# Kernel tuning notes

Hardware: AMD Instinct MI355X
Metric: run time of the kernel (lower is better)

Reference implementation:

```python
import jax, jax.numpy as jnp
import numpy as np

# Hyperparameters (from HOIMLoss init_kwargs / defaults)
NUM_PIDS = 5532
NUM_CQ = 5000
NUM_BG = 5000
NUM_FEATURES = 256
BATCH = 4096
OIM_SCALAR = 30.0
ALPHA_D = 0.25
ALPHA_R = 0.25
GAMMA_D = 2.0
GAMMA_R = 2.0


def _l2norm(x):
    return x / jnp.maximum(jnp.linalg.norm(x, axis=-1, keepdims=True), 1e-12)


def setup_inputs() -> dict:
    key = jax.random.key(0)
    k1, k2, k3, k4, k5 = jax.random.split(key, 5)
    inputs = _l2norm(jax.random.normal(k1, (BATCH, NUM_FEATURES), dtype=jnp.float32))
    # roi_label: -2 = background, -1 = ignored unlabeled, [0, NUM_PIDS) = identity
    roi_label = jax.random.randint(k2, (BATCH,), -2, NUM_PIDS)
    lut = _l2norm(jax.random.normal(k3, (NUM_PIDS, NUM_FEATURES), dtype=jnp.float32))
    cq = _l2norm(jax.random.normal(k4, (NUM_CQ, NUM_FEATURES), dtype=jnp.float32))
    cqb = _l2norm(jax.random.normal(k5, (NUM_BG, NUM_FEATURES), dtype=jnp.float32))
    return {"inputs": inputs, "roi_label": roi_label, "lut": lut, "cq": cq, "cqb": cqb}


def reference(inputs, roi_label, lut, cq, cqb):
    # OIM2CQ.forward: concat([inputs@cqb.T, inputs@lut.T, inputs@cq.T], dim=1)
    table = jnp.concatenate([cqb, lut, cq], axis=0)        # [BG+P+CQ, F]
    projected = OIM_SCALAR * (inputs @ table.T)            # [B, BG+P+CQ]

    valid = roi_label >= -1      # non-background rows (inds in torch code)
    labeled = roi_label >= 0     # rows contributing to nll (ignore_index=-1)

    # OIM focal loss over non-background columns [labeled | unlabeled]
    proj_non_bg = projected[:, NUM_BG:]                    # [B, P+CQ]
    logp = jax.nn.log_softmax(proj_non_bg, axis=-1)
    p = jnp.exp(logp)
    focal_p = ALPHA_R * (1.0 - p) ** GAMMA_R * logp
    safe_lab = jnp.clip(roi_label, 0, NUM_PIDS - 1)
    row_loss = -jnp.take_along_axis(focal_p, safe_lab[:, None], axis=1)[:, 0]
    row_loss = jnp.where(labeled, row_loss, 0.0)           # ignore_index=-1 -> 0

    # Detection focal loss over (background, foreground) mass
    all_probs = jax.nn.softmax(projected, axis=-1)
    cls_score = jnp.stack(
        [all_probs[:, :NUM_BG].sum(axis=-1), all_probs[:, NUM_BG:].sum(axis=-1)],
        axis=-1,
    )                                                      # [B, 2]
    det_label = jnp.clip(roi_label + 2, 0, 1)              # -2 -> 0, else 1
    focal_det = ALPHA_D * (1.0 - cls_score) ** GAMMA_D * jnp.log(cls_score)
    loss_det = -jnp.take_along_axis(focal_det, det_label[:, None], axis=1)[:, 0].mean()

    # dynamic_lambda: weight per-row oim loss by detached fg prob squared
    cls_non_bg = jax.lax.stop_gradient(cls_score[:, 1])
    row_loss = row_loss * cls_non_bg ** 2
    n_valid = jnp.maximum(valid.sum(), 1).astype(projected.dtype)
    loss_oim = jnp.sum(jnp.where(valid, row_loss, 0.0)) / n_valid

    return cls_score, loss_det, loss_oim
```

## Files before the change

kernel.cpp:

```cpp
#include <hip/hip_runtime.h>
#include <hip/hip_bf16.h>

typedef unsigned short u16;
typedef __attribute__((ext_vector_type(8))) short bf16x8;
typedef __attribute__((ext_vector_type(4))) short bf16x4;
typedef __attribute__((ext_vector_type(4))) float f32x4;
typedef __attribute__((ext_vector_type(16))) float f32x16;

#define NBG   5000
#define NPID  5532
#define NTOT  15532
#define FEAT  256
#define BATCH 4096
#define SCALE_LOG2E 43.280851226668994f
#define LPITCH 264

#define BGPAD    5120
#define TOTPAD   15872
#define NCHUNKS  62
#define NTILE_B  992
#define TILE_SH  4096
#define NTILE_A  256
#define STEP_SH  8192
#define NB_LIMIT 15652

#define TABT_BYTES ((size_t)NTILE_B * TILE_SH * 2)
#define AT_BYTES   ((size_t)NTILE_A * TILE_SH * 2)
#define SUMS_OFF   (TABT_BYTES + AT_BYTES)
#define SUMS_FLOATS 8196
#define WS_NEED    (SUMS_OFF + SUMS_FLOATS * 4)

__device__ __forceinline__ float fexp2(float x) {
#if __has_builtin(__builtin_amdgcn_exp2f)
    return __builtin_amdgcn_exp2f(x);
#else
    return exp2f(x);
#endif
}

__device__ __forceinline__ void atomic_add_f(float* p, float v) {
    __hip_atomic_fetch_add(p, v, __ATOMIC_RELAXED, __HIP_MEMORY_SCOPE_AGENT);
}
__device__ __forceinline__ short f2bf(float f) {
    return (short)__bfloat16_as_ushort(__float2bfloat16(f));
}
__device__ __forceinline__ int swz(int rc, int q) { return q ^ ((rc >> 1) & 3); }

__device__ __forceinline__ const float* table_row(
    int n, const float* __restrict__ lut, const float* __restrict__ cq,
    const float* __restrict__ cqb)
{
    const int nc = n < NTOT ? n : NTOT - 1;
    if (nc < NBG)        return cqb + (size_t)nc * FEAT;
    if (nc < NBG + NPID) return lut + (size_t)(nc - NBG) * FEAT;
    return cq + (size_t)(nc - NBG - NPID) * FEAT;
}

#define TAB_UNITS (NTILE_B * 512)
#define A_UNITS   (NTILE_A * 512)
#define PRE_BLOCKS ((TAB_UNITS + A_UNITS) / 256)

__global__ __launch_bounds__(256) void prepass_kernel(
    const float* __restrict__ inputs, const float* __restrict__ lut,
    const float* __restrict__ cq, const float* __restrict__ cqb,
    u16* __restrict__ tabt, u16* __restrict__ at, float* __restrict__ S)
{
    const int u = blockIdx.x * 256 + threadIdx.x;
    if (u < SUMS_FLOATS) S[u] = 0.f;

    if (u < TAB_UNITS) {
        const int tile = u >> 9, v = u & 511;
        const int kk = v >> 6, col = (v >> 2) & 15, q = v & 3;
        const int cg = tile * 16 + col;
        const int srcn  = (cg < BGPAD) ? cg : cg - 120;
        const bool valid = (cg < BGPAD) ? (cg < NBG) : (cg < NB_LIMIT);
        bf16x8 r = {0, 0, 0, 0, 0, 0, 0, 0};
        if (valid) {
            const float* src = table_row(srcn, lut, cq, cqb) + kk * 32 + q * 8;
            const f32x4 lo = *(const f32x4*)src;
            const f32x4 hi = *(const f32x4*)(src + 4);
            r = bf16x8{ f2bf(lo[0] * SCALE_LOG2E), f2bf(lo[1] * SCALE_LOG2E),
                        f2bf(lo[2] * SCALE_LOG2E), f2bf(lo[3] * SCALE_LOG2E),
                        f2bf(hi[0] * SCALE_LOG2E), f2bf(hi[1] * SCALE_LOG2E),
                        f2bf(hi[2] * SCALE_LOG2E), f2bf(hi[3] * SCALE_LOG2E) };
        }
        const size_t off = (size_t)tile * TILE_SH + kk * 512 + col * 32 + swz(col, q) * 8;
        *(bf16x8*)(tabt + off) = r;
    } else {
        const int ua = u - TAB_UNITS;
        const int tile = ua >> 9, v = ua & 511;
        const int kk = v >> 6, row = (v >> 2) & 15, q = v & 3;
        const float* src = inputs + (size_t)(tile * 16 + row) * FEAT + kk * 32 + q * 8;
        const f32x4 lo = *(const f32x4*)src;
        const f32x4 hi = *(const f32x4*)(src + 4);
        bf16x8 r = { f2bf(lo[0]), f2bf(lo[1]), f2bf(lo[2]), f2bf(lo[3]),
                     f2bf(hi[0]), f2bf(hi[1]), f2bf(hi[2]), f2bf(hi[3]) };
        const size_t off = (size_t)tile * TILE_SH + kk * 512 + row * 32 + swz(row, q) * 8;
        *(bf16x8*)(at + off) = r;
    }
}

__global__ __launch_bounds__(512)
__attribute__((amdgpu_waves_per_eu(4, 4)))
void score_bf16_kernel(
    const u16* __restrict__ tabt, const u16* __restrict__ at,
    float* __restrict__ sum_bg, float* __restrict__ sum_nb)
{
    __shared__ __align__(16) short lbuf[2][STEP_SH];
    const int lid = blockIdx.x;
    const int x8  = lid & 7;
    const int j   = lid >> 3;
    const int rowchunk = x8 * 2 + (j & 1);
    const int colchunk = j >> 1;

    const int tid  = threadIdx.x;
    const int wave = tid >> 6;
    const int lane = tid & 63;
    const int col5 = lane & 31;
    const int half = lane >> 5;
    const int l15  = lane & 15;
    const int tsel = (lane >> 4) & 1;
    const int s0 = l15 * 32 + swz(l15, half) * 8;
    const int s1 = l15 * 32 + swz(l15, 2 + half) * 8;

    const bool isbg  = colchunk < 20;
    const int  limit = isbg ? NBG : NB_LIMIT;
    const int  steps = (colchunk == 19) ? 5 : (colchunk == 61) ? 2 : 8;
    const int  maskstep = (colchunk == 19 || colchunk == 61) ? steps - 1 : 8;
    const u16* gbase = tabt + (size_t)colchunk * 16 * TILE_SH;

    const int stage_off = wave * 512 + lane * 8;
    #define STAGE(buf_, t_)                                                    \
        {                                                                      \
            const u16* gs = gbase + (size_t)(t_) * STEP_SH + stage_off;        \
            short* ls = &lbuf[buf_][wave * 512];                               \
            __builtin_amdgcn_global_load_lds(                                  \
                (const __attribute__((address_space(1))) void*)(gs),           \
                (__attribute__((address_space(3))) void*)(ls), 16, 0, 0);      \
            __builtin_amdgcn_global_load_lds(                                  \
                (const __attribute__((address_space(1))) void*)(gs + 4096),    \
                (__attribute__((address_space(3))) void*)(ls + 4096), 16, 0, 0); \
        }

    STAGE(0, 0);

    bf16x8 af[16];
    {
        const u16* ab = at + (size_t)(rowchunk * 16 + wave * 2 + tsel) * TILE_SH;
        #pragma unroll
        for (int ks = 0; ks < 16; ++ks)
            af[ks] = *(const bf16x8*)(ab + (ks >> 1) * 512 + ((ks & 1) ? s1 : s0));
    }

    float p[16];
    #pragma unroll
    for (int i = 0; i < 16; ++i) p[i] = 0.f;

    #pragma unroll 1
    for (int t = 0; t < steps; ++t) {
        __syncthreads();
        if (t + 1 < steps) STAGE((t + 1) & 1, t + 1);

        const short* lb = lbuf[t & 1] + tsel * TILE_SH;
        f32x16 acc = {};
        __builtin_amdgcn_s_setprio(1);
        #pragma unroll
        for (int ks = 0; ks < 16; ++ks) {
            const bf16x8 b = *(const bf16x8*)(lb + (ks >> 1) * 512 + ((ks & 1) ? s1 : s0));
            acc = __builtin_amdgcn_mfma_f32_32x32x16_bf16(af[ks], b, acc, 0, 0, 0);
        }
        __builtin_amdgcn_s_setprio(0);

        if (t == maskstep) {
            const bool okc = (colchunk * 256 + t * 32 + col5) < limit;
            #pragma unroll
            for (int i = 0; i < 16; ++i)
                p[i] += okc ? fexp2(acc[i]) : 0.f;
        } else {
            #pragma unroll
            for (int i = 0; i < 16; ++i)
                p[i] += fexp2(acc[i]);
        }
    }

    #pragma unroll
    for (int off = 1; off < 32; off <<= 1) {
        #pragma unroll
        for (int i = 0; i < 16; ++i)
            p[i] += __shfl_xor(p[i], off);
    }
    if (col5 == 0) {
        float* dst = isbg ? sum_bg : sum_nb;
        #pragma unroll
        for (int reg = 0; reg < 16; ++reg) {
            const int row = rowchunk * 256 + wave * 32
                          + (reg & 3) + 8 * (reg >> 2) + 4 * half;
            atomic_add_f(&dst[row], p[reg]);
        }
    }
    #undef STAGE
}

__global__ __launch_bounds__(256, 2) void score_f32_kernel(
    const float* __restrict__ inputs, const float* __restrict__ lut,
    const float* __restrict__ cq, const float* __restrict__ cqb,
    float* __restrict__ sum_bg, float* __restrict__ sum_nb)
{
    __shared__ __align__(16) short lds[32 * LPITCH];
    const int wave = threadIdx.x >> 6;
    const int lane = threadIdx.x & 63;
    const int l15  = lane & 15;
    const int quad = lane >> 4;
    const int rowbase = blockIdx.y * 256;
    const int colbase = blockIdx.x * 256;

    bf16x8 afrag[4][8];
    #pragma unroll 1
    for (int c = 0; c < 8; ++c) {
        __syncthreads();
        #pragma unroll
        for (int i = 0; i < 8; ++i) {
            const int lr = i * 4 + wave;
            const f32x4 v = *(const f32x4*)(inputs + (size_t)(rowbase + c * 32 + lr) * FEAT + lane * 4);
            bf16x4 h = { f2bf(v[0]), f2bf(v[1]), f2bf(v[2]), f2bf(v[3]) };
            *(bf16x4*)(&lds[lr * LPITCH + lane * 4]) = h;
        }
        __syncthreads();
        if ((c >> 1) == wave) {
            const int half = c & 1;
            #pragma unroll
            for (int j2 = 0; j2 < 2; ++j2) {
                const int lr = j2 * 16 + l15;
                #pragma unroll
                for (int kk = 0; kk < 8; ++kk)
                    afrag[half * 2 + j2][kk] =
                        *(const bf16x8*)(&lds[lr * LPITCH + kk * 32 + quad * 8]);
            }
        }
    }

    float pbg[16], pnb[16];
    #pragma unroll
    for (int i = 0; i < 16; ++i) { pbg[i] = 0.f; pnb[i] = 0.f; }

    #pragma unroll 1
    for (int s = 0; s < 8; ++s) {
        __syncthreads();
        #pragma unroll
        for (int i = 0; i < 8; ++i) {
            const int lc = i * 4 + wave;
            const f32x4 v = *(const f32x4*)(table_row(colbase + s * 32 + lc, lut, cq, cqb) + lane * 4);
            bf16x4 h = { f2bf(v[0]), f2bf(v[1]), f2bf(v[2]), f2bf(v[3]) };
            *(bf16x4*)(&lds[lc * LPITCH + lane * 4]) = h;
        }
        __syncthreads();

        #pragma unroll
        for (int st = 0; st < 2; ++st) {
            const int lc = st * 16 + l15;
            f32x4 cc[4];
            #pragma unroll
            for (int q = 0; q < 4; ++q) cc[q] = f32x4{0.f, 0.f, 0.f, 0.f};
            #pragma unroll
            for (int kk = 0; kk < 8; ++kk) {
                const bf16x8 b = *(const bf16x8*)(&lds[lc * LPITCH + kk * 32 + quad * 8]);
                cc[0] = __builtin_amdgcn_mfma_f32_16x16x32_bf16(afrag[0][kk], b, cc[0], 0, 0, 0);
                cc[1] = __builtin_amdgcn_mfma_f32_16x16x32_bf16(afrag[1][kk], b, cc[1], 0, 0, 0);
                cc[2] = __builtin_amdgcn_mfma_f32_16x16x32_bf16(afrag[2][kk], b, cc[2], 0, 0, 0);
                cc[3] = __builtin_amdgcn_mfma_f32_16x16x32_bf16(afrag[3][kk], b, cc[3], 0, 0, 0);
            }
            const int n = colbase + s * 32 + st * 16 + l15;
            const bool okc  = n < NTOT;
            const bool isbg = n < NBG;
            #pragma unroll
            for (int q = 0; q < 4; ++q) {
                #pragma unroll
                for (int r = 0; r < 4; ++r) {
                    float e = exp2f(cc[q][r] * SCALE_LOG2E);
                    e = okc ? e : 0.f;
                    pbg[q * 4 + r] += isbg ? e : 0.f;
                    pnb[q * 4 + r] += isbg ? 0.f : e;
                }
            }
        }
    }

    #pragma unroll
    for (int off = 1; off < 16; off <<= 1) {
        #pragma unroll
        for (int i = 0; i < 16; ++i) {
            pbg[i] += __shfl_xor(pbg[i], off);
            pnb[i] += __shfl_xor(pnb[i], off);
        }
    }
    if (l15 == 0) {
        #pragma unroll
        for (int q = 0; q < 4; ++q) {
            #pragma unroll
            for (int r = 0; r < 4; ++r) {
                const int row = rowbase + wave * 64 + q * 16 + quad * 4 + r;
                atomic_add_f(&sum_bg[row], pbg[q * 4 + r]);
                atomic_add_f(&sum_nb[row], pnb[q * 4 + r]);
            }
        }
    }
}

__global__ __launch_bounds__(256) void finalize_kernel(
    const float* __restrict__ inputs, const int* __restrict__ roi_label,
    const float* __restrict__ lut,
    const float* __restrict__ sum_bg, const float* __restrict__ sum_nb,
    float* __restrict__ accums, unsigned int* __restrict__ ticket,
    float* __restrict__ out)
{
    __shared__ float s_det[4], s_oim[4], s_nv[4];
    const int wid  = threadIdx.x >> 6;
    const int lane = threadIdx.x & 63;

    float det_a = 0.f, oim_a = 0.f, nv_a = 0.f;

    #pragma unroll 1
    for (int it = 0; it < 8; ++it) {
        const int row = blockIdx.x * 32 + wid * 8 + it;
        const int r   = roi_label[row];

        float dot = 0.f;
        {
            const int rc = r < 0 ? 0 : r;
            const f32x4 xi = *(const f32x4*)(inputs + (size_t)row * FEAT + lane * 4);
            const f32x4 li = *(const f32x4*)(lut + (size_t)rc * FEAT + lane * 4);
            #pragma unroll
            for (int jj = 0; jj < 4; ++jj) {
                float a = __bfloat162float(__float2bfloat16(xi[jj]));
                float b = __bfloat162float(__float2bfloat16(li[jj]));
                dot += a * b;
            }
        }
        #pragma unroll
        for (int off = 32; off > 0; off >>= 1) dot += __shfl_xor(dot, off);

        if (lane == 0) {
            const float sbg = sum_bg[row];
            const float snb = sum_nb[row];
            const float inv = 1.f / (sbg + snb);
            const float cls0 = sbg * inv;
            const float cls1 = snb * inv;
            out[2 * row]     = cls0;
            out[2 * row + 1] = cls1;

            const float cs = (r >= -1) ? cls1 : cls0;
            const float om = 1.f - cs;
            det_a += -(0.25f * om * om * logf(cs)) * (1.f / (float)BATCH);
            nv_a  += (r >= -1) ? 1.f : 0.f;

            if (r >= 0) {
                const float slab = 30.f * dot;
                const float logp = slab - logf(snb);
                const float p    = expf(logp);
                const float om2  = 1.f - p;
                oim_a += -(0.25f * om2 * om2 * logp) * cls1 * cls1;
            }
        }
    }

    if (lane == 0) { s_det[wid] = det_a; s_oim[wid] = oim_a; s_nv[wid] = nv_a; }
    __syncthreads();
    if (threadIdx.x == 0) {
        atomic_add_f(&accums[0], s_det[0] + s_det[1] + s_det[2] + s_det[3]);
        atomic_add_f(&accums[1], s_oim[0] + s_oim[1] + s_oim[2] + s_oim[3]);
        atomic_add_f(&accums[2], s_nv[0] + s_nv[1] + s_nv[2] + s_nv[3]);
        __threadfence();
        const unsigned t = __hip_atomic_fetch_add(ticket, 1u, __ATOMIC_ACQ_REL,
                                                  __HIP_MEMORY_SCOPE_AGENT);
        if (t == gridDim.x - 1) {
            const float det = __hip_atomic_load(&accums[0], __ATOMIC_RELAXED, __HIP_MEMORY_SCOPE_AGENT);
            const float oim = __hip_atomic_load(&accums[1], __ATOMIC_RELAXED, __HIP_MEMORY_SCOPE_AGENT);
            float nv        = __hip_atomic_load(&accums[2], __ATOMIC_RELAXED, __HIP_MEMORY_SCOPE_AGENT);
            if (nv < 1.f) nv = 1.f;
            out[2 * BATCH]     = det;
            out[2 * BATCH + 1] = oim / nv;
        }
    }
}

extern "C" void kernel_launch(void* const* d_in, const int* in_sizes, int n_in,
                              void* d_out, int out_size, void* d_ws, size_t ws_size,
                              hipStream_t stream)
{
    const float* inputs = (const float*)d_in[0];
    const int*   roi    = (const int*)d_in[1];
    const float* lut    = (const float*)d_in[2];
    const float* cq     = (const float*)d_in[3];
    const float* cqb    = (const float*)d_in[4];
    float* out = (float*)d_out;

    if (ws_size >= (size_t)WS_NEED) {
        u16* tabt = (u16*)d_ws;
        u16* at   = (u16*)((char*)d_ws + TABT_BYTES);
        float* S  = (float*)((char*)d_ws + SUMS_OFF);
        prepass_kernel<<<PRE_BLOCKS, 256, 0, stream>>>(inputs, lut, cq, cqb, tabt, at, S);
        score_bf16_kernel<<<992, 512, 0, stream>>>(tabt, at, S, S + BATCH);
        finalize_kernel<<<128, 256, 0, stream>>>(
            inputs, roi, lut, S, S + BATCH, S + 2 * BATCH,
            (unsigned int*)(S + 2 * BATCH + 3), out);
    } else {
        float* S = (float*)d_ws;
        hipMemsetAsync(S, 0, SUMS_FLOATS * sizeof(float), stream);
        dim3 g1(61, 16);
        score_f32_kernel<<<g1, 256, 0, stream>>>(inputs, lut, cq, cqb, S, S + BATCH);
        finalize_kernel<<<128, 256, 0, stream>>>(
            inputs, roi, lut, S, S + BATCH, S + 2 * BATCH,
            (unsigned int*)(S + 2 * BATCH + 3), out);
    }
}
```

Measured before the change: 135.8 us.

## Use linear fragment layout and defer exp of previous MFMA tile

Reorganizes the prepacked bf16 table and input buffers into 32-wide groups stored in MFMA fragment order, so each lane reads contiguous 16-byte chunks at lane*8 with no swizzle arithmetic. The exp2 accumulation for step t is deferred until after step t+1's MFMA chain is issued, so the transcendental work can overlap the matrix ops. The cost is holding an extra 16-float accumulator live per thread, which adds register pressure, and the linear LDS reads may see more bank conflicts now that the swizzle is gone.

```diff
diff --git a/kernel.cpp b/kernel.cpp
--- a/kernel.cpp
+++ b/kernel.cpp
@@ -17,15 +17,14 @@
 
 #define BGPAD    5120
 #define TOTPAD   15872
-#define NCHUNKS  62
-#define NTILE_B  992
-#define TILE_SH  4096
-#define NTILE_A  256
+#define NB_LIMIT 15652
+#define NGRP_B   496
+#define NGRP_A   128
+#define GRP_SH   8192
 #define STEP_SH  8192
-#define NB_LIMIT 15652
-
-#define TABT_BYTES ((size_t)NTILE_B * TILE_SH * 2)
-#define AT_BYTES   ((size_t)NTILE_A * TILE_SH * 2)
+
+#define TABT_BYTES ((size_t)NGRP_B * GRP_SH * 2)
+#define AT_BYTES   ((size_t)NGRP_A * GRP_SH * 2)
 #define SUMS_OFF   (TABT_BYTES + AT_BYTES)
 #define SUMS_FLOATS 8196
 #define WS_NEED    (SUMS_OFF + SUMS_FLOATS * 4)
@@ -44,7 +43,6 @@
 __device__ __forceinline__ short f2bf(float f) {
     return (short)__bfloat16_as_ushort(__float2bfloat16(f));
 }
-__device__ __forceinline__ int swz(int rc, int q) { return q ^ ((rc >> 1) & 3); }
 
 __device__ __forceinline__ const float* table_row(
     int n, const float* __restrict__ lut, const float* __restrict__ cq,
@@ -56,8 +54,8 @@
     return cq + (size_t)(nc - NBG - NPID) * FEAT;
 }
 
-#define TAB_UNITS (NTILE_B * 512)
-#define A_UNITS   (NTILE_A * 512)
+#define TAB_UNITS (NGRP_B * 1024)
+#define A_UNITS   (NGRP_A * 1024)
 #define PRE_BLOCKS ((TAB_UNITS + A_UNITS) / 256)
 
 __global__ __launch_bounds__(256) void prepass_kernel(
@@ -69,14 +67,14 @@
     if (u < SUMS_FLOATS) S[u] = 0.f;
 
     if (u < TAB_UNITS) {
-        const int tile = u >> 9, v = u & 511;
-        const int kk = v >> 6, col = (v >> 2) & 15, q = v & 3;
-        const int cg = tile * 16 + col;
+        const int g = u >> 10, ks = (u >> 6) & 15;
+        const int half = (u >> 5) & 1, c = u & 31;
+        const int cg = g * 32 + c;
         const int srcn  = (cg < BGPAD) ? cg : cg - 120;
         const bool valid = (cg < BGPAD) ? (cg < NBG) : (cg < NB_LIMIT);
         bf16x8 r = {0, 0, 0, 0, 0, 0, 0, 0};
         if (valid) {
-            const float* src = table_row(srcn, lut, cq, cqb) + kk * 32 + q * 8;
+            const float* src = table_row(srcn, lut, cq, cqb) + ks * 16 + half * 8;
             const f32x4 lo = *(const f32x4*)src;
             const f32x4 hi = *(const f32x4*)(src + 4);
             r = bf16x8{ f2bf(lo[0] * SCALE_LOG2E), f2bf(lo[1] * SCALE_LOG2E),
@@ -84,19 +82,17 @@
                         f2bf(hi[0] * SCALE_LOG2E), f2bf(hi[1] * SCALE_LOG2E),
                         f2bf(hi[2] * SCALE_LOG2E), f2bf(hi[3] * SCALE_LOG2E) };
         }
-        const size_t off = (size_t)tile * TILE_SH + kk * 512 + col * 32 + swz(col, q) * 8;
-        *(bf16x8*)(tabt + off) = r;
+        *(bf16x8*)(tabt + (size_t)u * 8) = r;
     } else {
         const int ua = u - TAB_UNITS;
-        const int tile = ua >> 9, v = ua & 511;
-        const int kk = v >> 6, row = (v >> 2) & 15, q = v & 3;
-        const float* src = inputs + (size_t)(tile * 16 + row) * FEAT + kk * 32 + q * 8;
+        const int g = ua >> 10, ks = (ua >> 6) & 15;
+        const int half = (ua >> 5) & 1, c = ua & 31;
+        const float* src = inputs + (size_t)(g * 32 + c) * FEAT + ks * 16 + half * 8;
         const f32x4 lo = *(const f32x4*)src;
         const f32x4 hi = *(const f32x4*)(src + 4);
         bf16x8 r = { f2bf(lo[0]), f2bf(lo[1]), f2bf(lo[2]), f2bf(lo[3]),
                      f2bf(hi[0]), f2bf(hi[1]), f2bf(hi[2]), f2bf(hi[3]) };
-        const size_t off = (size_t)tile * TILE_SH + kk * 512 + row * 32 + swz(row, q) * 8;
-        *(bf16x8*)(at + off) = r;
+        *(bf16x8*)(at + (size_t)ua * 8) = r;
     }
 }
 
@@ -118,16 +114,12 @@
     const int lane = tid & 63;
     const int col5 = lane & 31;
     const int half = lane >> 5;
-    const int l15  = lane & 15;
-    const int tsel = (lane >> 4) & 1;
-    const int s0 = l15 * 32 + swz(l15, half) * 8;
-    const int s1 = l15 * 32 + swz(l15, 2 + half) * 8;
 
     const bool isbg  = colchunk < 20;
     const int  limit = isbg ? NBG : NB_LIMIT;
     const int  steps = (colchunk == 19) ? 5 : (colchunk == 61) ? 2 : 8;
     const int  maskstep = (colchunk == 19 || colchunk == 61) ? steps - 1 : 8;
-    const u16* gbase = tabt + (size_t)colchunk * 16 * TILE_SH;
+    const u16* gbase = tabt + (size_t)colchunk * 8 * GRP_SH;
 
     const int stage_off = wave * 512 + lane * 8;
     #define STAGE(buf_, t_)                                                    \
@@ -142,46 +134,55 @@
                 (__attribute__((address_space(3))) void*)(ls + 4096), 16, 0, 0); \
         }
 
+    #define EXPACC(acc_, tp_)                                                  \
+        {                                                                      \
+            if ((tp_) == maskstep) {                                           \
+                const bool okc = (colchunk * 256 + (tp_) * 32 + col5) < limit; \
+                _Pragma("unroll")                                              \
+                for (int i_ = 0; i_ < 16; ++i_)                                \
+                    p[i_] += okc ? fexp2((acc_)[i_]) : 0.f;                    \
+            } else {                                                           \
+                _Pragma("unroll")                                              \
+                for (int i_ = 0; i_ < 16; ++i_)                                \
+                    p[i_] += fexp2((acc_)[i_]);                                \
+            }                                                                  \
+        }
+
     STAGE(0, 0);
 
     bf16x8 af[16];
     {
-        const u16* ab = at + (size_t)(rowchunk * 16 + wave * 2 + tsel) * TILE_SH;
+        const u16* ab = at + (size_t)(rowchunk * 8 + wave) * GRP_SH + lane * 8;
         #pragma unroll
         for (int ks = 0; ks < 16; ++ks)
-            af[ks] = *(const bf16x8*)(ab + (ks >> 1) * 512 + ((ks & 1) ? s1 : s0));
+            af[ks] = *(const bf16x8*)(ab + ks * 512);
     }
 
     float p[16];
     #pragma unroll
     for (int i = 0; i < 16; ++i) p[i] = 0.f;
+
+    f32x16 accP = {};
 
     #pragma unroll 1
     for (int t = 0; t < steps; ++t) {
         __syncthreads();
         if (t + 1 < steps) STAGE((t + 1) & 1, t + 1);
 
-        const short* lb = lbuf[t & 1] + tsel * TILE_SH;
+        const short* lb = lbuf[t & 1];
         f32x16 acc = {};
         __builtin_amdgcn_s_setprio(1);
         #pragma unroll
         for (int ks = 0; ks < 16; ++ks) {
-            const bf16x8 b = *(const bf16x8*)(lb + (ks >> 1) * 512 + ((ks & 1) ? s1 : s0));
+            const bf16x8 b = *(const bf16x8*)(lb + ks * 512 + lane * 8);
             acc = __builtin_amdgcn_mfma_f32_32x32x16_bf16(af[ks], b, acc, 0, 0, 0);
         }
         __builtin_amdgcn_s_setprio(0);
 
-        if (t == maskstep) {
-            const bool okc = (colchunk * 256 + t * 32 + col5) < limit;
-            #pragma unroll
-            for (int i = 0; i < 16; ++i)
-                p[i] += okc ? fexp2(acc[i]) : 0.f;
-        } else {
-            #pragma unroll
-            for (int i = 0; i < 16; ++i)
-                p[i] += fexp2(acc[i]);
-        }
-    }
+        if (t > 0) EXPACC(accP, t - 1);
+        accP = acc;
+    }
+    EXPACC(accP, steps - 1);
 
     #pragma unroll
     for (int off = 1; off < 32; off <<= 1) {
@@ -199,6 +200,7 @@
         }
     }
     #undef STAGE
+    #undef EXPACC
 }
 
 __global__ __launch_bounds__(256, 2) void score_f32_kernel(
```

Result: slower. 143.7 us (+5.8%).
